# Kernel optimization log

Measured on AMD Instinct MI355X. Metric: run time of the kernel, lower is better.

Reference implementation:

```python
import jax, jax.numpy as jnp
import numpy as np

# loss weights (module defaults)
LCLASS, LNOOBJ, LOBJ, LBOX = 1.0, 10.0, 1.0, 10.0


def setup_inputs() -> dict:
    key = jax.random.key(0)
    k1, k2, k3, k4 = jax.random.split(key, 4)
    B, A, S, D, N, NCLS = 32, 3, 52, 85, 20, 80  # D = 5 + NCLS
    X = jax.random.normal(k1, (B, A, S, S, D), dtype=jnp.float32)
    # normalized box centers/sizes in (0,1)
    yboxes = jax.random.uniform(k2, (B, N, 4), dtype=jnp.float32, minval=1e-3, maxval=0.999)
    ylabels = jax.random.randint(k3, (B, N), 0, NCLS).astype(jnp.int32)
    anchors = jax.random.uniform(k4, (A, 2), dtype=jnp.float32, minval=0.05, maxval=1.0)
    return {"X": X, "yboxes": yboxes, "ylabels": ylabels, "anchors": anchors, "nclasses": NCLS}


def reference(X, yboxes, ylabels, anchors, nclasses):
    # Faithful to the torch module: hgrid = X.shape[-3], wgrid = X.shape[-4].
    B, A = X.shape[0], anchors.shape[0]
    hgrid = X.shape[-3]
    wgrid = X.shape[-4]  # == A for X laid out [B, A, S, S, D] (original code's quirk)
    N = yboxes.shape[1]
    K = B * N

    boxes = yboxes.reshape(K, 4)           # [K,4] (x, y, w, h)
    labs = ylabels.reshape(K)              # [K]
    img = jnp.repeat(jnp.arange(B, dtype=jnp.int32), N)  # image index per box

    y = jnp.floor(boxes[:, 1] * hgrid).astype(jnp.int32)
    x = jnp.floor(boxes[:, 0] * wgrid).astype(jnp.int32)

    # `taken` is shared across the whole batch and a box claims ALL free anchors
    # at its cell (no break in the anchor loop). Hence only the globally-first
    # box hitting a cell contributes, with all A anchors.
    cell = y * wgrid + x                   # [K]
    order = jnp.arange(K, dtype=jnp.int32)
    BIG = jnp.int32(2 ** 30)
    first = jnp.full((hgrid * wgrid,), BIG, dtype=jnp.int32).at[cell].min(order)
    contrib = (first[cell] == order).astype(X.dtype)  # [K] 1.0 if this box contributes

    # Gather predictions for all anchors at each box's cell: [K, A, D]
    P = X[img, :, y, x, :]

    # objectness: BCEWithLogits vs target 1.0 -> softplus(-z)
    obj = jax.nn.softplus(-P[:, :, 0])     # [K, A]

    xrel = boxes[:, 0] * wgrid - x.astype(X.dtype)   # fractional cell offset
    yrel = boxes[:, 1] * hgrid - y.astype(X.dtype)
    w_c = boxes[:, 2][:, None] / anchors[None, :, 0]  # [K, A]
    h_c = boxes[:, 3][:, None] / anchors[None, :, 1]
    tgt = jnp.stack([
        jnp.broadcast_to(xrel[:, None], (K, A)),
        jnp.broadcast_to(yrel[:, None], (K, A)),
        w_c,
        h_c,
    ], axis=-1)                                        # [K, A, 4]
    boxl = jnp.mean((P[:, :, 1:5] - tgt) ** 2, axis=-1)  # MSE mean over 4 elems

    # classification: CE with one-hot target == -log_softmax[label]
    logp = jax.nn.log_softmax(P[:, :, 5:], axis=-1)    # [K, A, nclasses]
    idx = jnp.broadcast_to(labs[:, None, None], (K, A, 1)).astype(jnp.int32)
    clsl = -jnp.take_along_axis(logp, idx, axis=-1)[..., 0]  # [K, A]

    per = LOBJ * obj + LBOX * boxl + LCLASS * clsl     # [K, A]
    loss = jnp.sum(per.sum(axis=1) * contrib)
    return loss.reshape(1)
```

## Files before the change

### kernel.cpp

```cpp
#include <hip/hip_runtime.h>
#include <math.h>

#define BB    32
#define AA    3
#define SS    52
#define DD    85
#define NN    20
#define NCLS  80
#define KK    (BB * NN)
#define WGRID 3
#define HGRID 52
#define HW    (HGRID * WGRID)
#define BIGV  (1 << 30)
#define NEGINF (-__builtin_inff())


__global__ void __launch_bounds__(256)
yolo_prep_kernel(const float* __restrict__ yboxes,
                 int* __restrict__ ws,
                 float* __restrict__ out) {
    __shared__ int first[HW];
    __shared__ int cnt;
    const int tid = threadIdx.x;
    if (tid < HW) first[tid] = BIGV;
    if (tid == 0) cnt = 0;
    __syncthreads();

    const float4* __restrict__ b4 = (const float4*)yboxes;
    for (int k = tid; k < KK; k += 256) {
        float4 b = b4[k];
        int x = (int)floorf(b.x * (float)WGRID);
        int y = (int)floorf(b.y * (float)HGRID);
        atomicMin(&first[y * WGRID + x], k);
    }
    __syncthreads();

    if (tid < HW) {
        int f = first[tid];
        if (f < BIGV) {
            int slot = atomicAdd(&cnt, 1);
            ws[1 + slot] = f;
        }
    }
    __syncthreads();
    if (tid == 0) {
        ws[0] = cnt;
        out[0] = 0.0f;
    }
}

__global__ void __launch_bounds__(256)
yolo_loss_kernel(const float* __restrict__ X,
                 const float* __restrict__ yboxes,
                 const int* __restrict__ ylabels,
                 const float* __restrict__ anchors,
                 const int* __restrict__ ws,
                 float* __restrict__ out) {
    const int wave = (blockIdx.x * 256 + threadIdx.x) >> 6;
    const int lane = threadIdx.x & 63;

    const int cnt = ws[0];
    const int kidx = wave / 3;
    if (kidx >= cnt) return;
    const int a = wave - 3 * kidx;

    const int k = ws[1 + kidx];
    const float4 bb = ((const float4*)yboxes)[k];
    const int lab = ylabels[k];
    const float2 anc = ((const float2*)anchors)[a];

    const int x = (int)floorf(bb.x * (float)WGRID);
    const int y = (int)floorf(bb.y * (float)HGRID);
    const int img = k / NN;

    const float* __restrict__ P =
        X + ((((size_t)img * AA + a) * SS + y) * SS + x) * DD;

    float e0 = P[lane];
    float e1 = NEGINF;
    if (lane < 21) e1 = P[64 + lane];

    float v = fmaxf((lane >= 5) ? e0 : NEGINF, (lane < 21) ? e1 : NEGINF);
#pragma unroll
    for (int m = 1; m < 64; m <<= 1) v = fmaxf(v, __shfl_xor(v, m, 64));
    const float mx = v;

    float s = ((lane >= 5) ? expf(e0 - mx) : 0.0f) +
              ((lane < 21) ? expf(e1 - mx) : 0.0f);
#pragma unroll
    for (int m = 1; m < 64; m <<= 1) s += __shfl_xor(s, m, 64);

    const int idx = 5 + lab;
    const float plab = (idx < 64) ? __shfl(e0, idx, 64)
                                  : __shfl(e1, idx - 64, 64);

    const float p0 = __shfl(e0, 0, 64);
    const float p1 = __shfl(e0, 1, 64);
    const float p2 = __shfl(e0, 2, 64);
    const float p3 = __shfl(e0, 3, 64);
    const float p4 = __shfl(e0, 4, 64);

    const float z = -p0;
    const float obj = fmaxf(z, 0.0f) + log1pf(expf(-fabsf(z)));

    const float xrel = bb.x * (float)WGRID - (float)x;
    const float yrel = bb.y * (float)HGRID - (float)y;
    const float wc = bb.z / anc.x;
    const float hc = bb.w / anc.y;
    const float d1 = p1 - xrel, d2 = p2 - yrel, d3 = p3 - wc, d4 = p4 - hc;
    const float boxl = 0.25f * (d1 * d1 + d2 * d2 + d3 * d3 + d4 * d4);

    const float clsl = -(plab - mx - logf(s));

    const float per = obj + 10.0f * boxl + clsl;
    if (lane == 0) atomicAdd(out, per);
}

extern "C" void kernel_launch(void* const* d_in, const int* in_sizes, int n_in,
                              void* d_out, int out_size, void* d_ws, size_t ws_size,
                              hipStream_t stream) {
    const float* X       = (const float*)d_in[0];
    const float* yboxes  = (const float*)d_in[1];
    const int*   ylabels = (const int*)d_in[2];
    const float* anchors = (const float*)d_in[3];

    float* out = (float*)d_out;
    int*   ws  = (int*)d_ws;

    yolo_prep_kernel<<<1, 256, 0, stream>>>(yboxes, ws, out);

    yolo_loss_kernel<<<(HW * AA) / 4, 256, 0, stream>>>(X, yboxes, ylabels,
                                                        anchors, ws, out);
}
```

Baseline: 17.97 us.

## Fuse prep and loss kernels into one cooperative kernel with grid sync

New measurement: 39.48 us. +119.7%, slower.

```diff
diff --git a/kernel.cpp b/kernel.cpp
--- a/kernel.cpp
+++ b/kernel.cpp
@@ -1,5 +1,8 @@
 #include <hip/hip_runtime.h>
+#include <hip/hip_cooperative_groups.h>
 #include <math.h>
+
+namespace cg = cooperative_groups;
 
 #define BB    32
 #define AA    3
@@ -13,107 +16,107 @@
 #define HW    (HGRID * WGRID)
 #define BIGV  (1 << 30)
 #define NEGINF (-__builtin_inff())
-
+#define NTASK (HW * AA)
+#define NBLOCKS (NTASK / 4)
 
 __global__ void __launch_bounds__(256)
-yolo_prep_kernel(const float* __restrict__ yboxes,
-                 int* __restrict__ ws,
+yolo_coop_kernel(const float* __restrict__ X,
+                 const float* __restrict__ yboxes,
+                 const int* __restrict__ ylabels,
+                 const float* __restrict__ anchors,
+                 float* __restrict__ wsf,
                  float* __restrict__ out) {
-    __shared__ int first[HW];
-    __shared__ int cnt;
-    const int tid = threadIdx.x;
+    __shared__ float4 sbox[KK];
+    __shared__ int    first[HW];
+    __shared__ float  sred[4];
+
+    const int tid  = threadIdx.x;
+    const int lane = tid & 63;
+
     if (tid < HW) first[tid] = BIGV;
-    if (tid == 0) cnt = 0;
     __syncthreads();
-
     const float4* __restrict__ b4 = (const float4*)yboxes;
+#pragma unroll
     for (int k = tid; k < KK; k += 256) {
         float4 b = b4[k];
+        sbox[k] = b;
         int x = (int)floorf(b.x * (float)WGRID);
         int y = (int)floorf(b.y * (float)HGRID);
         atomicMin(&first[y * WGRID + x], k);
     }
     __syncthreads();
 
-    if (tid < HW) {
-        int f = first[tid];
-        if (f < BIGV) {
-            int slot = atomicAdd(&cnt, 1);
-            ws[1 + slot] = f;
-        }
+    const int w    = blockIdx.x * 4 + (tid >> 6);
+    const int cell = w / 3;
+    const int a    = w - 3 * cell;
+
+    float per = 0.0f;
+    const int k = first[cell];
+    if (k < BIGV) {
+        const float4 bb = sbox[k];
+        const int lab = ylabels[k];
+        const float2 anc = ((const float2*)anchors)[a];
+
+        const int x = (int)floorf(bb.x * (float)WGRID);
+        const int y = (int)floorf(bb.y * (float)HGRID);
+        const int img = k / NN;
+
+        const float* __restrict__ P =
+            X + ((((size_t)img * AA + a) * SS + y) * SS + x) * DD;
+
+        float e0 = P[lane];
+        float e1 = (lane < 21) ? P[64 + lane] : NEGINF;
+
+        float v = fmaxf((lane >= 5) ? e0 : NEGINF, (lane < 21) ? e1 : NEGINF);
+#pragma unroll
+        for (int m = 1; m < 64; m <<= 1) v = fmaxf(v, __shfl_xor(v, m, 64));
+        const float mx = v;
+
+        float s = ((lane >= 5) ? expf(e0 - mx) : 0.0f) +
+                  ((lane < 21) ? expf(e1 - mx) : 0.0f);
+#pragma unroll
+        for (int m = 1; m < 64; m <<= 1) s += __shfl_xor(s, m, 64);
+
+        const int idx = 5 + lab;
+        const float plab = (idx < 64) ? __shfl(e0, idx, 64)
+                                      : __shfl(e1, idx - 64, 64);
+
+        const float p0 = __shfl(e0, 0, 64);
+        const float p1 = __shfl(e0, 1, 64);
+        const float p2 = __shfl(e0, 2, 64);
+        const float p3 = __shfl(e0, 3, 64);
+        const float p4 = __shfl(e0, 4, 64);
+
+        const float z = -p0;
+        const float obj = fmaxf(z, 0.0f) + log1pf(expf(-fabsf(z)));
+
+        const float xrel = bb.x * (float)WGRID - (float)x;
+        const float yrel = bb.y * (float)HGRID - (float)y;
+        const float wc = bb.z / anc.x;
+        const float hc = bb.w / anc.y;
+        const float d1 = p1 - xrel, d2 = p2 - yrel;
+        const float d3 = p3 - wc,   d4 = p4 - hc;
+        const float boxl = 0.25f * (d1 * d1 + d2 * d2 + d3 * d3 + d4 * d4);
+
+        const float clsl = -(plab - mx - logf(s));
+
+        per = obj + 10.0f * boxl + clsl;
     }
-    __syncthreads();
-    if (tid == 0) {
-        ws[0] = cnt;
-        out[0] = 0.0f;
+    if (lane == 0) wsf[w] = per;
+    __threadfence();
+
+    cg::this_grid().sync();
+
+    if (blockIdx.x == 0) {
+        float v = wsf[tid];
+        const int t2 = tid + 256;
+        if (t2 < NTASK) v += wsf[t2];
+#pragma unroll
+        for (int off = 32; off > 0; off >>= 1) v += __shfl_down(v, off, 64);
+        if (lane == 0) sred[tid >> 6] = v;
+        __syncthreads();
+        if (tid == 0) out[0] = sred[0] + sred[1] + sred[2] + sred[3];
     }
-}
-
-__global__ void __launch_bounds__(256)
-yolo_loss_kernel(const float* __restrict__ X,
-                 const float* __restrict__ yboxes,
-                 const int* __restrict__ ylabels,
-                 const float* __restrict__ anchors,
-                 const int* __restrict__ ws,
-                 float* __restrict__ out) {
-    const int wave = (blockIdx.x * 256 + threadIdx.x) >> 6;
-    const int lane = threadIdx.x & 63;
-
-    const int cnt = ws[0];
-    const int kidx = wave / 3;
-    if (kidx >= cnt) return;
-    const int a = wave - 3 * kidx;
-
-    const int k = ws[1 + kidx];
-    const float4 bb = ((const float4*)yboxes)[k];
-    const int lab = ylabels[k];
-    const float2 anc = ((const float2*)anchors)[a];
-
-    const int x = (int)floorf(bb.x * (float)WGRID);
-    const int y = (int)floorf(bb.y * (float)HGRID);
-    const int img = k / NN;
-
-    const float* __restrict__ P =
-        X + ((((size_t)img * AA + a) * SS + y) * SS + x) * DD;
-
-    float e0 = P[lane];
-    float e1 = NEGINF;
-    if (lane < 21) e1 = P[64 + lane];
-
-    float v = fmaxf((lane >= 5) ? e0 : NEGINF, (lane < 21) ? e1 : NEGINF);
-#pragma unroll
-    for (int m = 1; m < 64; m <<= 1) v = fmaxf(v, __shfl_xor(v, m, 64));
-    const float mx = v;
-
-    float s = ((lane >= 5) ? expf(e0 - mx) : 0.0f) +
-              ((lane < 21) ? expf(e1 - mx) : 0.0f);
-#pragma unroll
-    for (int m = 1; m < 64; m <<= 1) s += __shfl_xor(s, m, 64);
-
-    const int idx = 5 + lab;
-    const float plab = (idx < 64) ? __shfl(e0, idx, 64)
-                                  : __shfl(e1, idx - 64, 64);
-
-    const float p0 = __shfl(e0, 0, 64);
-    const float p1 = __shfl(e0, 1, 64);
-    const float p2 = __shfl(e0, 2, 64);
-    const float p3 = __shfl(e0, 3, 64);
-    const float p4 = __shfl(e0, 4, 64);
-
-    const float z = -p0;
-    const float obj = fmaxf(z, 0.0f) + log1pf(expf(-fabsf(z)));
-
-    const float xrel = bb.x * (float)WGRID - (float)x;
-    const float yrel = bb.y * (float)HGRID - (float)y;
-    const float wc = bb.z / anc.x;
-    const float hc = bb.w / anc.y;
-    const float d1 = p1 - xrel, d2 = p2 - yrel, d3 = p3 - wc, d4 = p4 - hc;
-    const float boxl = 0.25f * (d1 * d1 + d2 * d2 + d3 * d3 + d4 * d4);
-
-    const float clsl = -(plab - mx - logf(s));
-
-    const float per = obj + 10.0f * boxl + clsl;
-    if (lane == 0) atomicAdd(out, per);
 }
 
 extern "C" void kernel_launch(void* const* d_in, const int* in_sizes, int n_in,
@@ -125,10 +128,10 @@
     const float* anchors = (const float*)d_in[3];
 
     float* out = (float*)d_out;
-    int*   ws  = (int*)d_ws;
+    float* wsf = (float*)d_ws;
 
-    yolo_prep_kernel<<<1, 256, 0, stream>>>(yboxes, ws, out);
-
-    yolo_loss_kernel<<<(HW * AA) / 4, 256, 0, stream>>>(X, yboxes, ylabels,
-                                                        anchors, ws, out);
+    void* args[] = { (void*)&X, (void*)&yboxes, (void*)&ylabels,
+                     (void*)&anchors, (void*)&wsf, (void*)&out };
+    hipLaunchCooperativeKernel((const void*)yolo_coop_kernel,
+                               dim3(NBLOCKS), dim3(256), args, 0, stream);
 }
```
